# Kernel tuning notes

Hardware: AMD Instinct MI355X
Metric: run time of the kernel (lower is better)

Reference implementation:

```python
import jax, jax.numpy as jnp
import numpy as np

N, V, NF, EF, EMB, OUT, MP = 512, 40, 32, 4, 128, 128, 3
BIG_NEG = -1.0e6


def _build_graph():
    """Build a batch of random molecule-like graphs (path + extra edges, one-hot
    bond features) and replicate the torch index-construction logic in numpy."""
    rng = np.random.default_rng(0)
    edges = np.zeros((N, V, V, EF), np.float32)
    perm = np.argsort(rng.random((N, V)), axis=1)
    b = np.repeat(np.arange(N), V - 1)
    i = perm[:, :-1].ravel(); j = perm[:, 1:].ravel()
    t = rng.integers(0, EF, b.shape)
    edges[b, i, j, t] = 1.0; edges[b, j, i, t] = 1.0
    NEX = 6  # extra edges per graph
    u = rng.integers(0, V, (N, NEX))
    v = rng.integers(0, V - 1, (N, NEX)); v = v + (v >= u)  # no self loops
    b2 = np.repeat(np.arange(N), NEX); t2 = rng.integers(0, EF, b2.shape)
    edges[b2, u.ravel(), v.ravel(), t2] = 1.0; edges[b2, v.ravel(), u.ravel(), t2] = 1.0
    # keep edge features strictly one-hot (adjacency = edges.sum(-1) must be 0/1)
    multi = edges.sum(-1) > 1
    edges = np.where(multi[..., None], np.eye(EF, dtype=np.float32)[edges.argmax(-1)], edges)

    adj = (edges.sum(-1) > 0).astype(np.float32)            # (N,V,V) binary
    b_idx, n_idx, nb_idx = np.nonzero(adj)                  # directed edge list, row-major
    E = b_idx.shape[0]
    adj_e = np.zeros((N, V, V), np.int64)
    adj_e[b_idx, n_idx, nb_idx] = np.arange(1, E + 1)       # edge-id+1 in adjacency slots
    rows = adj_e[b_idx, nb_idx, :]                          # (E,V): edges into each edge's nghb
    deg = (rows > 0).sum(1)
    eb = rows[rows > 0] - 1                                 # ingoing edge ids (row-major = torch cat order)
    igeb = np.repeat(np.arange(E), deg)                     # receiving-edge index
    ige = np.arange(deg.sum()) - np.repeat(np.cumsum(deg) - deg, deg)  # slot within receiver
    keep = n_idx[igeb] != nb_idx[eb]                        # drop the reverse edge
    eb, igeb, ige = eb[keep], igeb[keep], ige[keep]
    D = int(adj.sum(-1).max())                              # max node degree
    mask = np.zeros((E, D), np.float32); mask[igeb, ige] = 1.0
    node_mask = (adj.sum(-1) > 0).astype(np.float32)        # (N,V)
    return edges, b_idx, n_idx, nb_idx, eb, igeb, ige, mask, node_mask


def setup_inputs() -> dict:
    edges, b_idx, n_idx, nb_idx, eb, igeb, ige, mask, node_mask = _build_graph()
    key = jax.random.key(0)
    ks = jax.random.split(key, 8)
    def lin(k, fi, fo):
        return (jax.random.normal(k, (fi, fo), jnp.float32) / np.sqrt(fi)).astype(jnp.float32)
    return dict(
        nodes=jax.random.normal(ks[0], (N, V, NF), jnp.float32),
        edges=jnp.asarray(edges),
        W_pre=lin(ks[1], 2 * NF + EF, EMB), b_pre=jnp.zeros((EMB,), jnp.float32),
        W_att=lin(ks[2], 2 * EMB, EMB), b_att=jnp.zeros((EMB,), jnp.float32),
        W_emb=lin(ks[3], 2 * EMB, EMB), b_emb=jnp.zeros((EMB,), jnp.float32),
        Wg_att=lin(ks[4], 2 * EMB, EMB), bg_att=jnp.zeros((EMB,), jnp.float32),
        Wg_emb=lin(ks[5], EMB, EMB), bg_emb=jnp.zeros((EMB,), jnp.float32),
        W_out=lin(ks[6], EMB, OUT), b_out=jnp.zeros((OUT,), jnp.float32),
        ingoing_mask=jnp.asarray(mask), node_mask=jnp.asarray(node_mask),
        eb_b=jnp.asarray(b_idx, jnp.int32), eb_n=jnp.asarray(n_idx, jnp.int32),
        eb_nb=jnp.asarray(nb_idx, jnp.int32),
        in_eb=jnp.asarray(eb, jnp.int32), in_igeb=jnp.asarray(igeb, jnp.int32),
        in_ige=jnp.asarray(ige, jnp.int32),
    )


def reference(nodes, edges, W_pre, b_pre, W_att, b_att, W_emb, b_emb,
              Wg_att, bg_att, Wg_emb, bg_emb, W_out, b_out,
              ingoing_mask, node_mask, eb_b, eb_n, eb_nb, in_eb, in_igeb, in_ige):
    E, D = ingoing_mask.shape
    # preprocess_edges (EMN): tanh MLP on [node, neighbour, edge] per directed edge
    e_in = jnp.concatenate([nodes[eb_b, eb_n], nodes[eb_b, eb_nb],
                            edges[eb_b, eb_n, eb_nb]], axis=-1)        # (E, 2NF+EF)
    e_emb = jnp.tanh(e_in @ W_pre + b_pre)                              # (E, EMB)
    energy_mask = (1.0 - ingoing_mask)[:, :, None] * BIG_NEG            # (E, D, 1)
    e_bcast = jnp.broadcast_to(e_emb[:, None, :], (E, D, EMB))

    def step(mem, _):
        # scatter ingoing edge memories into padded (E, D, EMB) slots, then
        # attention-aggregate (propagate_edges of EMN)
        in_mem = jnp.zeros((E, D, EMB), mem.dtype).at[in_igeb, in_ige].set(mem[in_eb])
        cat = jnp.concatenate([e_bcast, in_mem], axis=-1)               # (E, D, 2EMB)
        att = jax.nn.softmax(cat @ W_att + b_att + energy_mask, axis=1)
        msg = jnp.tanh(cat @ W_emb + b_emb)
        return (att * msg).sum(1), None

    mem0 = jnp.zeros((E, EMB), nodes.dtype)
    mem, _ = jax.lax.scan(step, mem0, None, length=MP)                  # (E, EMB)
    # node_sets scatter + sum over degree slots == segment-sum per (graph, node)
    graph_sets = jax.ops.segment_sum(mem, eb_b * V + eb_n,
                                     num_segments=N * V).reshape(N, V, EMB)
    # readout: attention GraphGather + dense head
    cat3 = jnp.concatenate([graph_sets, graph_sets], axis=-1)           # hidden == input
    g_att = jax.nn.softmax(cat3 @ Wg_att + bg_att +
                           (1.0 - node_mask)[:, :, None] * BIG_NEG, axis=1)
    g_emb = jnp.tanh(graph_sets @ Wg_emb + bg_emb)
    graph_embedding = (g_att * g_emb).sum(1)                            # (N, EMB)
    return graph_embedding @ W_out + b_out                              # (N, OUT)
```

## Files before the change

kernel.cpp:

```cpp
#include <hip/hip_runtime.h>
#include <hip/hip_bf16.h>
#include <math.h>

#define NN 512
#define VN 40
#define NF 32
#define EFD 4
#define OUTD 128
#define EMAX 96
#define DMAX 8
#define MSTR 136
#define WPSTR 104
#define NT 512
#define NW 8
#define EPW 12

typedef __attribute__((ext_vector_type(8))) short short8;
typedef __attribute__((ext_vector_type(4))) float f32x4;

__device__ __forceinline__ float fast_tanh(float x) {
    return fmaf(-2.0f, __builtin_amdgcn_rcpf(__expf(2.0f * x) + 1.0f), 1.0f);
}
__device__ __forceinline__ unsigned bf16b(float x) {
    __hip_bfloat16 h = __float2bfloat16(x);
    unsigned short u;
    __builtin_memcpy(&u, &h, 2);
    return (unsigned)u;
}

__global__ __launch_bounds__(256) void k_setup(
    const int* __restrict__ igeb, const int* __restrict__ eb_b,
    const float* __restrict__ W_att, const float* __restrict__ W_emb,
    const float* __restrict__ Wg_att, const float* __restrict__ Wg_emb,
    const float* __restrict__ W_pre,
    int* __restrict__ off, int* __restrict__ eoff,
    __hip_bfloat16* __restrict__ Wt1, __hip_bfloat16* __restrict__ Wt2,
    __hip_bfloat16* __restrict__ Wt3, __hip_bfloat16* __restrict__ Wpt,
    int K, int E, int nbO, int nbK)
{
    int bid = blockIdx.x, tid = threadIdx.x;
    if (bid < nbO) {
        int e = bid * 256 + tid;
        if (e >= E) return;
        int b = eb_b[e];
        if (e == 0) { for (int bb = 0; bb <= b; ++bb) off[bb] = 0; }
        else { int pb = eb_b[e - 1]; for (int bb = pb + 1; bb <= b; ++bb) off[bb] = e; }
        if (e == E - 1) { for (int bb = b + 1; bb <= NN; ++bb) off[bb] = E; }
        return;
    }
    bid -= nbO;
    if (bid < nbK) {
        int k = bid * 256 + tid;
        if (k >= K) return;
        int e = igeb[k];
        if (k == 0) { for (int ee = 0; ee <= e; ++ee) eoff[ee] = 0; }
        else { int pe = igeb[k - 1]; for (int ee = pe + 1; ee <= e; ++ee) eoff[ee] = k; }
        if (k == K - 1) { for (int ee = e + 1; ee <= E; ++ee) eoff[ee] = K; }
        return;
    }
    bid -= nbK;
    int c = bid * 2 + (tid >> 7), k = tid & 127;
    int cc = c & 127; bool hi = c >= 128;
    if (!hi) {
        Wt1[c * 128 + k] = __float2bfloat16(W_emb[k * 128 + c]);
        if (k < WPSTR)
            Wpt[c * WPSTR + k] = __float2bfloat16(k < 68 ? W_pre[k * 128 + c] : 0.f);
    }
    Wt2[c * 128 + k] = __float2bfloat16(hi ? W_emb[(128 + k) * 128 + cc] : W_att[(128 + k) * 128 + cc]);
    Wt3[c * 128 + k] = __float2bfloat16(hi ? Wg_emb[k * 128 + cc]
                                           : (Wg_att[k * 128 + cc] + Wg_att[(128 + k) * 128 + cc]));
}

__global__ __launch_bounds__(NT, 4) void k_mp(
    const float* __restrict__ nodes, const float* __restrict__ edges,
    const __hip_bfloat16* __restrict__ Wpt, const float* __restrict__ b_pre,
    const __hip_bfloat16* __restrict__ Wt1, const float* __restrict__ b_emb,
    const __hip_bfloat16* __restrict__ Wt2, const __hip_bfloat16* __restrict__ Wt3,
    const float* __restrict__ bg_att, const float* __restrict__ bg_emb,
    const int* __restrict__ igeb, const int* __restrict__ ieb,
    const int* __restrict__ eoff,
    const int* __restrict__ eb_n, const int* __restrict__ eb_nb,
    const float* __restrict__ node_mask,
    const float* __restrict__ W_out, const float* __restrict__ b_out,
    const int* __restrict__ off, float* __restrict__ out)
{
    __shared__ __align__(16) char pool[75264];
    __shared__ float gembL[128];
    __shared__ float nmL[VN];
    __shared__ int srcL[EMAX * DMAX];
    __shared__ int degL[EMAX];
    __shared__ int nodeL[EMAX];
    __shared__ int nbL[EMAX];
    __hip_bfloat16* eIn  = (__hip_bfloat16*)(pool + 26112);
    __hip_bfloat16* eL   = (__hip_bfloat16*)pool;
    __hip_bfloat16* beL  = (__hip_bfloat16*)(pool + 26112);
    const unsigned short* beLu = (const unsigned short*)(pool + 26112);
    const unsigned* beLw = (const unsigned*)(pool + 26112);
    __hip_bfloat16* memL = (__hip_bfloat16*)pool;
    unsigned*       MaMeL = (unsigned*)(pool + 26112);
    float*          nsF   = (float*)pool;
    __hip_bfloat16* nsbL  = (__hip_bfloat16*)(pool + 26112);
    unsigned*       GOLp  = (unsigned*)(pool + 39168);
    float*          numP  = (float*)pool;
    float*          denP  = (float*)(pool + 2048);
    float*          redL  = (float*)(pool + 4096);

    int b = blockIdx.x;
    int s0 = off[b], s1 = off[b + 1];
    int nE = s1 - s0;
    int tid = threadIdx.x;
    int wave = tid >> 6, lane = tid & 63, lm = lane & 15, lq = lane >> 4;

    if (tid < EMAX) {
        degL[tid] = 0;
        bool vld = tid < nE;
        int n = 0, nb = 0;
        if (vld) { n = eb_n[s0 + tid]; nb = eb_nb[s0 + tid]; }
        nodeL[tid] = n; nbL[tid] = nb;
        float4 ev = make_float4(0.f, 0.f, 0.f, 0.f);
        if (vld) ev = *(const float4*)&edges[(((size_t)b * VN + n) * VN + nb) * EFD];
        __hip_bfloat16* dst = &eIn[tid * WPSTR + 64];
        dst[0] = __float2bfloat16(ev.x);
        dst[1] = __float2bfloat16(ev.y);
        dst[2] = __float2bfloat16(ev.z);
        dst[3] = __float2bfloat16(ev.w);
        for (int f = 68; f < 96; ++f) eIn[tid * WPSTR + f] = __float2bfloat16(0.f);
    }
    if (tid < VN) nmL[tid] = node_mask[b * VN + tid];
    __syncthreads();
    for (int idx = tid; idx < EMAX * 16; idx += NT) {
        int le = idx >> 4, seg = idx & 15;
        float4 v4 = make_float4(0.f, 0.f, 0.f, 0.f);
        if (le < nE) {
            int node = (seg < 8) ? nodeL[le] : nbL[le];
            v4 = *(const float4*)&nodes[((size_t)b * VN + node) * NF + (seg & 7) * 4];
        }
        __hip_bfloat16* dst = &eIn[le * WPSTR + ((seg < 8) ? 0 : 32) + (seg & 7) * 4];
        dst[0] = __float2bfloat16(v4.x);
        dst[1] = __float2bfloat16(v4.y);
        dst[2] = __float2bfloat16(v4.z);
        dst[3] = __float2bfloat16(v4.w);
    }
    {
        int k0 = eoff[s0], k1 = eoff[s1];
        for (int k = k0 + tid; k < k1; k += NT) {
            int le = igeb[k] - s0;
            int pos = atomicAdd(&degL[le], 1);
            srcL[le * DMAX + pos] = ieb[k] - s0;
        }
    }
    __syncthreads();
    for (int t = wave; t < 48; t += NW) {
        int r = t >> 3, c = t & 7;
        short8 Af[3], Bf[3];
        #pragma unroll
        for (int kb = 0; kb < 3; ++kb) {
            Af[kb] = *(const short8*)((const short*)eIn + (r * 16 + lm) * WPSTR + kb * 32 + lq * 8);
            Bf[kb] = *(const short8*)((const short*)Wpt + (size_t)(c * 16 + lm) * WPSTR + kb * 32 + lq * 8);
        }
        f32x4 acc = {0.f, 0.f, 0.f, 0.f};
        #pragma unroll
        for (int kb = 0; kb < 3; ++kb)
            acc = __builtin_amdgcn_mfma_f32_16x16x32_bf16(Af[kb], Bf[kb], acc, 0, 0, 0);
        int col = c * 16 + lm;
        float bp = b_pre[col];
        #pragma unroll
        for (int i = 0; i < 4; ++i)
            eL[(r * 16 + lq * 4 + i) * MSTR + col] = __float2bfloat16(fast_tanh(acc[i] + bp));
    }
    __syncthreads();
    for (int t = wave; t < 48; t += NW) {
        int r = t >> 3, c = t & 7;
        short8 Af[4], Bf[4];
        #pragma unroll
        for (int kb = 0; kb < 4; ++kb) {
            Af[kb] = *(const short8*)((const short*)eL + (r * 16 + lm) * MSTR + kb * 32 + lq * 8);
            Bf[kb] = *(const short8*)((const short*)Wt1 + (size_t)(c * 16 + lm) * 128 + kb * 32 + lq * 8);
        }
        f32x4 acc = {0.f, 0.f, 0.f, 0.f};
        #pragma unroll
        for (int kb = 0; kb < 4; ++kb)
            acc = __builtin_amdgcn_mfma_f32_16x16x32_bf16(Af[kb], Bf[kb], acc, 0, 0, 0);
        int col = c * 16 + lm;
        float bv = b_emb[col];
        #pragma unroll
        for (int i = 0; i < 4; ++i)
            beL[(r * 16 + lq * 4 + i) * 128 + col] = __float2bfloat16(__expf(2.f * (acc[i] + bv)));
    }
    __syncthreads();
    unsigned e2bP[EPW];
    #pragma unroll
    for (int i = 0; i < EPW; ++i) {
        int le = wave + i * NW;
        unsigned lo = beLu[le * 128 + lane];
        unsigned hi = beLu[le * 128 + 64 + lane];
        e2bP[i] = (hi << 16) | lo;
    }
    for (int idx = tid; idx < EMAX * 64; idx += NT) {
        int le = idx >> 6, cp = idx & 63;
        unsigned pk = 0;
        if (le < nE) {
            unsigned w = beLw[le * 64 + cp];
            float e0 = __uint_as_float(w << 16);
            float e1 = __uint_as_float(w & 0xFFFF0000u);
            float v0 = fmaf(-2.f, __builtin_amdgcn_rcpf(e0 + 1.f), 1.f);
            float v1 = fmaf(-2.f, __builtin_amdgcn_rcpf(e1 + 1.f), 1.f);
            pk = (bf16b(v1) << 16) | bf16b(v0);
        }
        *(unsigned*)((unsigned short*)memL + le * MSTR + cp * 2) = pk;
    }
    __syncthreads();

    for (int step = 0; step < 2; ++step) {
        for (int p = wave; p < 48; p += NW) {
            int r = p >> 3, c = p & 7;
            short8 Af[4], Bf[4];
            #pragma unroll
            for (int kb = 0; kb < 4; ++kb) {
                Af[kb] = *(const short8*)((const short*)memL + (r * 16 + lm) * MSTR + kb * 32 + lq * 8);
                Bf[kb] = *(const short8*)((const short*)Wt2 + (size_t)(c * 16 + lm) * 128 + kb * 32 + lq * 8);
            }
            f32x4 aa = {0.f, 0.f, 0.f, 0.f};
            #pragma unroll
            for (int kb = 0; kb < 4; ++kb)
                aa = __builtin_amdgcn_mfma_f32_16x16x32_bf16(Af[kb], Bf[kb], aa, 0, 0, 0);
            #pragma unroll
            for (int kb = 0; kb < 4; ++kb)
                Bf[kb] = *(const short8*)((const short*)Wt2 + (size_t)(128 + c * 16 + lm) * 128 + kb * 32 + lq * 8);
            f32x4 ae = {0.f, 0.f, 0.f, 0.f};
            #pragma unroll
            for (int kb = 0; kb < 4; ++kb)
                ae = __builtin_amdgcn_mfma_f32_16x16x32_bf16(Af[kb], Bf[kb], ae, 0, 0, 0);
            int col = c * 16 + lm, row0 = r * 16 + lq * 4;
            #pragma unroll
            for (int i = 0; i < 4; ++i)
                MaMeL[(row0 + i) * 128 + col] =
                    (bf16b(__expf(2.f * ae[i])) << 16) | bf16b(__expf(aa[i]));
        }
        __syncthreads();
        if (step == 1) {
            for (int idx = tid; idx < VN * 128; idx += NT) nsF[idx] = 0.f;
            __syncthreads();
        }
        #pragma unroll
        for (int i = 0; i < EPW; ++i) {
            int le = wave + i * NW;
            if (le < nE) {
                int deg = __builtin_amdgcn_readfirstlane(degL[le]);
                int sv = srcL[le * DMAX + (lane & 7)];
                unsigned pkb = e2bP[i];
                float e2b0 = __uint_as_float(pkb << 16);
                float e2b1 = __uint_as_float(pkb & 0xFFFF0000u);
                float sw0 = 0.f, swr0 = 0.f, sw1 = 0.f, swr1 = 0.f;
                for (int d = 0; d < deg; ++d) {
                    int ls = __builtin_amdgcn_readlane(sv, d);
                    unsigned pk0 = MaMeL[ls * 128 + lane];
                    unsigned pk1 = MaMeL[ls * 128 + 64 + lane];
                    float w0 = __uint_as_float(pk0 << 16);
                    float m0 = __uint_as_float(pk0 & 0xFFFF0000u);
                    float w1 = __uint_as_float(pk1 << 16);
                    float m1 = __uint_as_float(pk1 & 0xFFFF0000u);
                    sw0 += w0;
                    swr0 = fmaf(w0, __builtin_amdgcn_rcpf(fmaf(e2b0, m0, 1.f)), swr0);
                    sw1 += w1;
                    swr1 = fmaf(w1, __builtin_amdgcn_rcpf(fmaf(e2b1, m1, 1.f)), swr1);
                }
                float r0 = deg ? swr0 * __builtin_amdgcn_rcpf(sw0)
                               : __builtin_amdgcn_rcpf(e2b0 + 1.f);
                float r1 = deg ? swr1 * __builtin_amdgcn_rcpf(sw1)
                               : __builtin_amdgcn_rcpf(e2b1 + 1.f);
                float v0 = fmaf(-2.f, r0, 1.f);
                float v1 = fmaf(-2.f, r1, 1.f);
                if (step == 0) {
                    memL[le * MSTR + lane] = __float2bfloat16(v0);
                    memL[le * MSTR + 64 + lane] = __float2bfloat16(v1);
                } else {
                    int v = __builtin_amdgcn_readfirstlane(nodeL[le]);
                    atomicAdd(&nsF[v * 128 + lane], v0);
                    atomicAdd(&nsF[v * 128 + 64 + lane], v1);
                }
            }
        }
        __syncthreads();
    }

    for (int idx = tid; idx < 48 * 128; idx += NT) {
        int v = idx >> 7, k = idx & 127;
        nsbL[v * MSTR + k] = __float2bfloat16(v < VN ? nsF[idx] : 0.f);
    }
    __syncthreads();
    for (int t = wave; t < 48; t += NW) {
        int r = t >> 4;
        int col0 = (t & 15) * 16;
        short8 Af[4], Bg[4];
        #pragma unroll
        for (int kb = 0; kb < 4; ++kb) {
            Af[kb] = *(const short8*)((const short*)nsbL + (r * 16 + lm) * MSTR + kb * 32 + lq * 8);
            Bg[kb] = *(const short8*)((const short*)Wt3 + (size_t)(col0 + lm) * 128 + kb * 32 + lq * 8);
        }
        f32x4 acc = {0.f, 0.f, 0.f, 0.f};
        #pragma unroll
        for (int kb = 0; kb < 4; ++kb)
            acc = __builtin_amdgcn_mfma_f32_16x16x32_bf16(Af[kb], Bg[kb], acc, 0, 0, 0);
        int col = col0 + lm;
        int cc = col & 127;
        float bv = (col < 128) ? bg_att[col] : bg_emb[cc];
        __hip_bfloat16* hp = (__hip_bfloat16*)GOLp;
        if (col < 128) {
            #pragma unroll
            for (int i2 = 0; i2 < 4; ++i2)
                hp[((r * 16 + lq * 4 + i2) * 128 + cc) * 2] =
                    __float2bfloat16(__expf(acc[i2] + bv));
        } else {
            #pragma unroll
            for (int i2 = 0; i2 < 4; ++i2)
                hp[((r * 16 + lq * 4 + i2) * 128 + cc) * 2 + 1] =
                    __float2bfloat16(__expf(2.f * (acc[i2] + bv)));
        }
    }
    __syncthreads();
    {
        int c = tid & 127, q = tid >> 7;
        float sw = 0.f, swr = 0.f;
        for (int v = q; v < VN; v += 4) {
            if (nmL[v] == 0.f) continue;
            unsigned pk = GOLp[v * 128 + c];
            float w = __uint_as_float(pk << 16);
            float e2 = __uint_as_float(pk & 0xFFFF0000u);
            sw += w;
            swr = fmaf(w, __builtin_amdgcn_rcpf(e2 + 1.f), swr);
        }
        numP[tid] = swr;
        denP[tid] = sw;
    }
    __syncthreads();
    if (tid < 128) {
        float swr = 0.f, sw = 0.f;
        #pragma unroll
        for (int p = 0; p < 4; ++p) { swr += numP[p * 128 + tid]; sw += denP[p * 128 + tid]; }
        gembL[tid] = fmaf(-2.f, swr / sw, 1.f);
    }
    __syncthreads();
    {
        int c = tid & 127, h = tid >> 7;
        float acc = 0.f;
        for (int j = h; j < 128; j += 4)
            acc += gembL[j] * W_out[j * OUTD + c];
        redL[tid] = acc;
    }
    __syncthreads();
    if (tid < 128) {
        float acc = b_out[tid];
        #pragma unroll
        for (int p = 0; p < 4; ++p) acc += redL[p * 128 + tid];
        out[(size_t)b * OUTD + tid] = acc;
    }
}

extern "C" void kernel_launch(void* const* d_in, const int* in_sizes, int n_in,
                              void* d_out, int out_size, void* d_ws, size_t ws_size,
                              hipStream_t stream) {
    const float* nodes    = (const float*)d_in[0];
    const float* edges    = (const float*)d_in[1];
    const float* W_pre    = (const float*)d_in[2];
    const float* b_pre    = (const float*)d_in[3];
    const float* W_att    = (const float*)d_in[4];
    const float* W_emb    = (const float*)d_in[6];
    const float* b_emb    = (const float*)d_in[7];
    const float* Wg_att   = (const float*)d_in[8];
    const float* bg_att   = (const float*)d_in[9];
    const float* Wg_emb   = (const float*)d_in[10];
    const float* bg_emb   = (const float*)d_in[11];
    const float* W_out    = (const float*)d_in[12];
    const float* b_out    = (const float*)d_in[13];
    const float* node_mask = (const float*)d_in[15];
    const int* eb_b   = (const int*)d_in[16];
    const int* eb_n   = (const int*)d_in[17];
    const int* eb_nb  = (const int*)d_in[18];
    const int* in_eb  = (const int*)d_in[19];
    const int* in_igeb = (const int*)d_in[20];

    int E = in_sizes[16];
    int K = in_sizes[19];

    __hip_bfloat16* Wt1 = (__hip_bfloat16*)d_ws;
    __hip_bfloat16* Wt2 = Wt1 + 128 * 128;
    __hip_bfloat16* Wt3 = Wt2 + 256 * 128;
    __hip_bfloat16* Wpt = Wt3 + 256 * 128;
    int* off  = (int*)(Wpt + 128 * WPSTR);
    int* eoff = off + (NN + 1);

    int nbO = (E + 255) / 256;
    int nbK = (K + 255) / 256;

    k_setup<<<nbO + nbK + 128, 256, 0, stream>>>(in_igeb, eb_b,
                                                 W_att, W_emb, Wg_att, Wg_emb, W_pre,
                                                 off, eoff, Wt1, Wt2, Wt3, Wpt,
                                                 K, E, nbO, nbK);
    k_mp<<<NN, NT, 0, stream>>>(nodes, edges, Wpt, b_pre, Wt1, b_emb,
                                Wt2, Wt3, bg_att, bg_emb,
                                in_igeb, in_eb, eoff, eb_n, eb_nb, node_mask,
                                W_out, b_out, off, (float*)d_out);
}
```

Baseline: 176.9 us.

## Hoist per-wave weight fragments into registers and fuse tanh into embed GEMM epilogue

```diff
diff --git a/kernel.cpp b/kernel.cpp
--- a/kernel.cpp
+++ b/kernel.cpp
@@ -26,6 +26,9 @@
     unsigned short u;
     __builtin_memcpy(&u, &h, 2);
     return (unsigned)u;
+}
+__device__ __forceinline__ unsigned packbf(float lo, float hi) {
+    return (bf16b(hi) << 16) | bf16b(lo);
 }
 
 __global__ __launch_bounds__(256) void k_setup(
@@ -95,7 +98,6 @@
     __hip_bfloat16* eL   = (__hip_bfloat16*)pool;
     __hip_bfloat16* beL  = (__hip_bfloat16*)(pool + 26112);
     const unsigned short* beLu = (const unsigned short*)(pool + 26112);
-    const unsigned* beLw = (const unsigned*)(pool + 26112);
     __hip_bfloat16* memL = (__hip_bfloat16*)pool;
     unsigned*       MaMeL = (unsigned*)(pool + 26112);
     float*          nsF   = (float*)pool;
@@ -119,12 +121,11 @@
         nodeL[tid] = n; nbL[tid] = nb;
         float4 ev = make_float4(0.f, 0.f, 0.f, 0.f);
         if (vld) ev = *(const float4*)&edges[(((size_t)b * VN + n) * VN + nb) * EFD];
-        __hip_bfloat16* dst = &eIn[tid * WPSTR + 64];
-        dst[0] = __float2bfloat16(ev.x);
-        dst[1] = __float2bfloat16(ev.y);
-        dst[2] = __float2bfloat16(ev.z);
-        dst[3] = __float2bfloat16(ev.w);
-        for (int f = 68; f < 96; ++f) eIn[tid * WPSTR + f] = __float2bfloat16(0.f);
+        unsigned* dst = (unsigned*)&eIn[tid * WPSTR + 64];
+        dst[0] = packbf(ev.x, ev.y);
+        dst[1] = packbf(ev.z, ev.w);
+        #pragma unroll
+        for (int f = 0; f < 14; ++f) dst[2 + f] = 0u;
     }
     if (tid < VN) nmL[tid] = node_mask[b * VN + tid];
     __syncthreads();
@@ -135,11 +136,9 @@
             int node = (seg < 8) ? nodeL[le] : nbL[le];
             v4 = *(const float4*)&nodes[((size_t)b * VN + node) * NF + (seg & 7) * 4];
         }
-        __hip_bfloat16* dst = &eIn[le * WPSTR + ((seg < 8) ? 0 : 32) + (seg & 7) * 4];
-        dst[0] = __float2bfloat16(v4.x);
-        dst[1] = __float2bfloat16(v4.y);
-        dst[2] = __float2bfloat16(v4.z);
-        dst[3] = __float2bfloat16(v4.w);
+        unsigned* dst = (unsigned*)&eIn[le * WPSTR + ((seg < 8) ? 0 : 32) + (seg & 7) * 4];
+        dst[0] = packbf(v4.x, v4.y);
+        dst[1] = packbf(v4.z, v4.w);
     }
     {
         int k0 = eoff[s0], k1 = eoff[s1];
@@ -150,44 +149,71 @@
         }
     }
     __syncthreads();
-    for (int t = wave; t < 48; t += NW) {
-        int r = t >> 3, c = t & 7;
-        short8 Af[3], Bf[3];
-        #pragma unroll
-        for (int kb = 0; kb < 3; ++kb) {
-            Af[kb] = *(const short8*)((const short*)eIn + (r * 16 + lm) * WPSTR + kb * 32 + lq * 8);
+    {
+        int c = wave;
+        short8 Bf[3];
+        #pragma unroll
+        for (int kb = 0; kb < 3; ++kb)
             Bf[kb] = *(const short8*)((const short*)Wpt + (size_t)(c * 16 + lm) * WPSTR + kb * 32 + lq * 8);
-        }
-        f32x4 acc = {0.f, 0.f, 0.f, 0.f};
-        #pragma unroll
-        for (int kb = 0; kb < 3; ++kb)
-            acc = __builtin_amdgcn_mfma_f32_16x16x32_bf16(Af[kb], Bf[kb], acc, 0, 0, 0);
+        float bp = b_pre[c * 16 + lm];
         int col = c * 16 + lm;
-        float bp = b_pre[col];
-        #pragma unroll
-        for (int i = 0; i < 4; ++i)
-            eL[(r * 16 + lq * 4 + i) * MSTR + col] = __float2bfloat16(fast_tanh(acc[i] + bp));
-    }
-    __syncthreads();
-    for (int t = wave; t < 48; t += NW) {
-        int r = t >> 3, c = t & 7;
-        short8 Af[4], Bf[4];
-        #pragma unroll
-        for (int kb = 0; kb < 4; ++kb) {
-            Af[kb] = *(const short8*)((const short*)eL + (r * 16 + lm) * MSTR + kb * 32 + lq * 8);
+        for (int r = 0; r < 6; ++r) {
+            short8 Af[3];
+            #pragma unroll
+            for (int kb = 0; kb < 3; ++kb)
+                Af[kb] = *(const short8*)((const short*)eIn + (r * 16 + lm) * WPSTR + kb * 32 + lq * 8);
+            f32x4 acc = {0.f, 0.f, 0.f, 0.f};
+            #pragma unroll
+            for (int kb = 0; kb < 3; ++kb)
+                acc = __builtin_amdgcn_mfma_f32_16x16x32_bf16(Af[kb], Bf[kb], acc, 0, 0, 0);
+            #pragma unroll
+            for (int i = 0; i < 4; ++i)
+                eL[(r * 16 + lq * 4 + i) * MSTR + col] = __float2bfloat16(fast_tanh(acc[i] + bp));
+        }
+    }
+    __syncthreads();
+    unsigned tnh[12];
+    {
+        int c = wave;
+        short8 Bf[4];
+        #pragma unroll
+        for (int kb = 0; kb < 4; ++kb)
             Bf[kb] = *(const short8*)((const short*)Wt1 + (size_t)(c * 16 + lm) * 128 + kb * 32 + lq * 8);
-        }
-        f32x4 acc = {0.f, 0.f, 0.f, 0.f};
-        #pragma unroll
-        for (int kb = 0; kb < 4; ++kb)
-            acc = __builtin_amdgcn_mfma_f32_16x16x32_bf16(Af[kb], Bf[kb], acc, 0, 0, 0);
+        float bv = b_emb[c * 16 + lm];
         int col = c * 16 + lm;
-        float bv = b_emb[col];
-        #pragma unroll
-        for (int i = 0; i < 4; ++i)
-            beL[(r * 16 + lq * 4 + i) * 128 + col] = __float2bfloat16(__expf(2.f * (acc[i] + bv)));
-    }
-    __syncthreads();
+        for (int r = 0; r < 6; ++r) {
+            short8 Af[4];
+            #pragma unroll
+            for (int kb = 0; kb < 4; ++kb)
+                Af[kb] = *(const short8*)((const short*)eL + (r * 16 + lm) * MSTR + kb * 32 + lq * 8);
+            f32x4 acc = {0.f, 0.f, 0.f, 0.f};
+            #pragma unroll
+            for (int kb = 0; kb < 4; ++kb)
+                acc = __builtin_amdgcn_mfma_f32_16x16x32_bf16(Af[kb], Bf[kb], acc, 0, 0, 0);
+            #pragma unroll
+            for (int i = 0; i < 4; ++i) {
+                int row = r * 16 + lq * 4 + i;
+                float e2 = __expf(2.f * (acc[i] + bv));
+                beL[row * 128 + col] = __float2bfloat16(e2);
+                unsigned tb = bf16b(fmaf(-2.f, __builtin_amdgcn_rcpf(e2 + 1.f), 1.f));
+                if (i & 1) tnh[r * 2 + (i >> 1)] |= tb << 16;
+                else       tnh[r * 2 + (i >> 1)]  = tb;
+            }
+        }
+    }
+    __syncthreads();
+    {
+        int col = wave * 16 + lm;
+        #pragma unroll
+        for (int r = 0; r < 6; ++r)
+            #pragma unroll
+            for (int i = 0; i < 4; ++i) {
+                int row = r * 16 + lq * 4 + i;
+                unsigned pk = tnh[r * 2 + (i >> 1)];
+                ((unsigned short*)memL)[row * MSTR + col] =
+                    (unsigned short)((i & 1) ? (pk >> 16) : (pk & 0xFFFFu));
+            }
+    }
     unsigned e2bP[EPW];
     #pragma unroll
     for (int i = 0; i < EPW; ++i) {
@@ -196,46 +222,40 @@
         unsigned hi = beLu[le * 128 + 64 + lane];
         e2bP[i] = (hi << 16) | lo;
     }
-    for (int idx = tid; idx < EMAX * 64; idx += NT) {
-        int le = idx >> 6, cp = idx & 63;
-        unsigned pk = 0;
-        if (le < nE) {
-            unsigned w = beLw[le * 64 + cp];
-            float e0 = __uint_as_float(w << 16);
-            float e1 = __uint_as_float(w & 0xFFFF0000u);
-            float v0 = fmaf(-2.f, __builtin_amdgcn_rcpf(e0 + 1.f), 1.f);
-            float v1 = fmaf(-2.f, __builtin_amdgcn_rcpf(e1 + 1.f), 1.f);
-            pk = (bf16b(v1) << 16) | bf16b(v0);
-        }
-        *(unsigned*)((unsigned short*)memL + le * MSTR + cp * 2) = pk;
-    }
-    __syncthreads();
+    __syncthreads();
+
+    short8 BfA[4], BfE[4];
+    {
+        int c = wave;
+        #pragma unroll
+        for (int kb = 0; kb < 4; ++kb) {
+            BfA[kb] = *(const short8*)((const short*)Wt2 + (size_t)(c * 16 + lm) * 128 + kb * 32 + lq * 8);
+            BfE[kb] = *(const short8*)((const short*)Wt2 + (size_t)(128 + c * 16 + lm) * 128 + kb * 32 + lq * 8);
+        }
+    }
 
     for (int step = 0; step < 2; ++step) {
-        for (int p = wave; p < 48; p += NW) {
-            int r = p >> 3, c = p & 7;
-            short8 Af[4], Bf[4];
-            #pragma unroll
-            for (int kb = 0; kb < 4; ++kb) {
-                Af[kb] = *(const short8*)((const short*)memL + (r * 16 + lm) * MSTR + kb * 32 + lq * 8);
-                Bf[kb] = *(const short8*)((const short*)Wt2 + (size_t)(c * 16 + lm) * 128 + kb * 32 + lq * 8);
-            }
-            f32x4 aa = {0.f, 0.f, 0.f, 0.f};
-            #pragma unroll
-            for (int kb = 0; kb < 4; ++kb)
-                aa = __builtin_amdgcn_mfma_f32_16x16x32_bf16(Af[kb], Bf[kb], aa, 0, 0, 0);
-            #pragma unroll
-            for (int kb = 0; kb < 4; ++kb)
-                Bf[kb] = *(const short8*)((const short*)Wt2 + (size_t)(128 + c * 16 + lm) * 128 + kb * 32 + lq * 8);
-            f32x4 ae = {0.f, 0.f, 0.f, 0.f};
-            #pragma unroll
-            for (int kb = 0; kb < 4; ++kb)
-                ae = __builtin_amdgcn_mfma_f32_16x16x32_bf16(Af[kb], Bf[kb], ae, 0, 0, 0);
-            int col = c * 16 + lm, row0 = r * 16 + lq * 4;
-            #pragma unroll
-            for (int i = 0; i < 4; ++i)
-                MaMeL[(row0 + i) * 128 + col] =
-                    (bf16b(__expf(2.f * ae[i])) << 16) | bf16b(__expf(aa[i]));
+        {
+            int col = wave * 16 + lm;
+            for (int r = 0; r < 6; ++r) {
+                short8 Af[4];
+                #pragma unroll
+                for (int kb = 0; kb < 4; ++kb)
+                    Af[kb] = *(const short8*)((const short*)memL + (r * 16 + lm) * MSTR + kb * 32 + lq * 8);
+                f32x4 aa = {0.f, 0.f, 0.f, 0.f};
+                #pragma unroll
+                for (int kb = 0; kb < 4; ++kb)
+                    aa = __builtin_amdgcn_mfma_f32_16x16x32_bf16(Af[kb], BfA[kb], aa, 0, 0, 0);
+                f32x4 ae = {0.f, 0.f, 0.f, 0.f};
+                #pragma unroll
+                for (int kb = 0; kb < 4; ++kb)
+                    ae = __builtin_amdgcn_mfma_f32_16x16x32_bf16(Af[kb], BfE[kb], ae, 0, 0, 0);
+                int row0 = r * 16 + lq * 4;
+                #pragma unroll
+                for (int i = 0; i < 4; ++i)
+                    MaMeL[(row0 + i) * 128 + col] =
+                        (bf16b(__expf(2.f * ae[i])) << 16) | bf16b(__expf(aa[i]));
+            }
         }
         __syncthreads();
         if (step == 1) {
@@ -284,38 +304,48 @@
         __syncthreads();
     }
 
-    for (int idx = tid; idx < 48 * 128; idx += NT) {
-        int v = idx >> 7, k = idx & 127;
-        nsbL[v * MSTR + k] = __float2bfloat16(v < VN ? nsF[idx] : 0.f);
-    }
-    __syncthreads();
-    for (int t = wave; t < 48; t += NW) {
-        int r = t >> 4;
-        int col0 = (t & 15) * 16;
-        short8 Af[4], Bg[4];
+    for (int idx = tid; idx < 48 * 64; idx += NT) {
+        int v = idx >> 6, kp = idx & 63;
+        unsigned pk = 0;
+        if (v < VN) pk = packbf(nsF[v * 128 + kp * 2], nsF[v * 128 + kp * 2 + 1]);
+        *(unsigned*)((unsigned short*)nsbL + v * MSTR + kp * 2) = pk;
+    }
+    __syncthreads();
+    {
+        int c0 = wave * 2, c1 = wave * 2 + 1;
+        short8 Bg0[4], Bg1[4];
         #pragma unroll
         for (int kb = 0; kb < 4; ++kb) {
-            Af[kb] = *(const short8*)((const short*)nsbL + (r * 16 + lm) * MSTR + kb * 32 + lq * 8);
-            Bg[kb] = *(const short8*)((const short*)Wt3 + (size_t)(col0 + lm) * 128 + kb * 32 + lq * 8);
-        }
-        f32x4 acc = {0.f, 0.f, 0.f, 0.f};
-        #pragma unroll
-        for (int kb = 0; kb < 4; ++kb)
-            acc = __builtin_amdgcn_mfma_f32_16x16x32_bf16(Af[kb], Bg[kb], acc, 0, 0, 0);
-        int col = col0 + lm;
-        int cc = col & 127;
-        float bv = (col < 128) ? bg_att[col] : bg_emb[cc];
+            Bg0[kb] = *(const short8*)((const short*)Wt3 + (size_t)(c0 * 16 + lm) * 128 + kb * 32 + lq * 8);
+            Bg1[kb] = *(const short8*)((const short*)Wt3 + (size_t)(c1 * 16 + lm) * 128 + kb * 32 + lq * 8);
+        }
+        int col0 = c0 * 16 + lm, col1 = c1 * 16 + lm;
+        float bv0 = (col0 < 128) ? bg_att[col0] : bg_emb[col0 & 127];
+        float bv1 = (col1 < 128) ? bg_att[col1] : bg_emb[col1 & 127];
         __hip_bfloat16* hp = (__hip_bfloat16*)GOLp;
-        if (col < 128) {
-            #pragma unroll
-            for (int i2 = 0; i2 < 4; ++i2)
-                hp[((r * 16 + lq * 4 + i2) * 128 + cc) * 2] =
-                    __float2bfloat16(__expf(acc[i2] + bv));
-        } else {
-            #pragma unroll
-            for (int i2 = 0; i2 < 4; ++i2)
-                hp[((r * 16 + lq * 4 + i2) * 128 + cc) * 2 + 1] =
-                    __float2bfloat16(__expf(2.f * (acc[i2] + bv)));
+        for (int r = 0; r < 3; ++r) {
+            short8 Af[4];
+            #pragma unroll
+            for (int kb = 0; kb < 4; ++kb)
+                Af[kb] = *(const short8*)((const short*)nsbL + (r * 16 + lm) * MSTR + kb * 32 + lq * 8);
+            f32x4 a0 = {0.f, 0.f, 0.f, 0.f}, a1 = {0.f, 0.f, 0.f, 0.f};
+            #pragma unroll
+            for (int kb = 0; kb < 4; ++kb) {
+                a0 = __builtin_amdgcn_mfma_f32_16x16x32_bf16(Af[kb], Bg0[kb], a0, 0, 0, 0);
+                a1 = __builtin_amdgcn_mfma_f32_16x16x32_bf16(Af[kb], Bg1[kb], a1, 0, 0, 0);
+            }
+            int row0 = r * 16 + lq * 4;
+            #pragma unroll
+            for (int i = 0; i < 4; ++i) {
+                if (col0 < 128)
+                    hp[((row0 + i) * 128 + col0) * 2] = __float2bfloat16(__expf(a0[i] + bv0));
+                else
+                    hp[((row0 + i) * 128 + (col0 & 127)) * 2 + 1] = __float2bfloat16(__expf(2.f * (a0[i] + bv0)));
+                if (col1 < 128)
+                    hp[((row0 + i) * 128 + col1) * 2] = __float2bfloat16(__expf(a1[i] + bv1));
+                else
+                    hp[((row0 + i) * 128 + (col1 & 127)) * 2 + 1] = __float2bfloat16(__expf(2.f * (a1[i] + bv1)));
+            }
         }
     }
     __syncthreads();
```

Result: slower. 185.9 us (+5.1%).
